# Optimization experiments

Measured on AMD Instinct MI355X. Metric: run time of the kernel, lower is better.

## Reference

```python
import jax, jax.numpy as jnp
import numpy as np

B, S, E = 2, 2048, 2048
H, D = 16, 128  # num_attention_heads, head_dim = hidden_size // num_heads


def rotate_half(x):
    x1 = x[..., : x.shape[-1] // 2]
    x2 = x[..., x.shape[-1] // 2 :]
    return jnp.concatenate((-x2, x1), axis=-1)


def setup_inputs() -> dict:
    key = jax.random.key(0)
    ks = jax.random.split(key, 7)
    return {
        "hidden_states": jax.random.normal(ks[0], (B, S, E), dtype=jnp.float32),
        "cos": jax.random.uniform(ks[1], (1, 1, S, D), dtype=jnp.float32),
        "sin": jax.random.uniform(ks[2], (1, 1, S, D), dtype=jnp.float32),
        "wq": jax.random.normal(ks[3], (E, H * D), dtype=jnp.float32) / np.sqrt(E),
        "wk": jax.random.normal(ks[4], (E, H * D), dtype=jnp.float32) / np.sqrt(E),
        "wv": jax.random.normal(ks[5], (E, H * D), dtype=jnp.float32) / np.sqrt(E),
        "wo": jax.random.normal(ks[6], (H * D, E), dtype=jnp.float32) / np.sqrt(H * D),
    }


def reference(hidden_states, cos, sin, wq, wk, wv, wo):
    # QKV projections (no bias, per attention_bias=False)
    q = (hidden_states @ wq).reshape(B, S, H, D).transpose(0, 2, 1, 3)  # bhsd
    k = (hidden_states @ wk).reshape(B, S, H, D).transpose(0, 2, 1, 3)
    v = (hidden_states @ wv).reshape(B, S, H, D).transpose(0, 2, 1, 3)
    # RoPE (applied after the head transpose, as in the original)
    q = q * cos + rotate_half(q) * sin
    k = k * cos + rotate_half(k) * sin
    # NOTE: original forward never applies self.scaling and uses no causal mask.
    scores = jnp.einsum("bhqd,bhkd->bhqk", q, k)
    attn = jax.nn.softmax(scores.astype(jnp.float32), axis=-1)
    out = jnp.einsum("bhqk,bhkd->bhqd", attn, v)
    out = out.transpose(0, 2, 1, 3).reshape(B, S, H * D)
    return out @ wo
```

## Files before the change

kernel.cpp:

```cpp
#include <hip/hip_runtime.h>
#include <stdint.h>

typedef _Float16 f16;
typedef _Float16 half8 __attribute__((ext_vector_type(8)));
typedef _Float16 half4 __attribute__((ext_vector_type(4)));
typedef __fp16 fp16x2 __attribute__((ext_vector_type(2)));
typedef float f32x4 __attribute__((ext_vector_type(4)));
typedef float f32x16 __attribute__((ext_vector_type(16)));
typedef uint32_t u32x4 __attribute__((ext_vector_type(4)));

static constexpr int Bsz = 2, S = 2048, E = 2048, H = 16, D = 128;
static constexpr int M = Bsz * S;
static constexpr int N_QKV = 3 * H * D;
static constexpr int HD = H * D;

__device__ __forceinline__ void gload_lds16(const void* gp, void* lp) {
  __builtin_amdgcn_global_load_lds(
      (const __attribute__((address_space(1))) uint32_t*)(uintptr_t)gp,
      (__attribute__((address_space(3))) uint32_t*)(uint32_t)(uintptr_t)lp,
      16, 0, 0);
}

__device__ __forceinline__ uint32_t pkrtz(float a, float b) {
  fp16x2 r = __builtin_amdgcn_cvt_pkrtz(a, b);
  return __builtin_bit_cast(uint32_t, r);
}

__global__ void cast_f32_f16(const float* __restrict__ in, f16* __restrict__ out) {
  size_t i = (size_t)(blockIdx.x * 256 + threadIdx.x) * 8;
  float4 a = *(const float4*)&in[i];
  float4 b = *(const float4*)&in[i + 4];
  half8 h;
  h[0] = (f16)a.x; h[1] = (f16)a.y; h[2] = (f16)a.z; h[3] = (f16)a.w;
  h[4] = (f16)b.x; h[5] = (f16)b.y; h[6] = (f16)b.z; h[7] = (f16)b.w;
  *(half8*)&out[i] = h;
}

__global__ void transpose_cast(const float* __restrict__ wq, const float* __restrict__ wk,
                               const float* __restrict__ wv, const float* __restrict__ wo,
                               f16* __restrict__ wt, f16* __restrict__ wot) {
  __shared__ float tile[32][33];
  int z = blockIdx.z;
  const float* src = (z == 0) ? wq : (z == 1) ? wk : (z == 2) ? wv : wo;
  f16* dst = (z == 3) ? wot : wt + (size_t)z * E * HD;
  int bx = blockIdx.x * 32, by = blockIdx.y * 32;
  int tx = threadIdx.x, ty = threadIdx.y;
#pragma unroll
  for (int r = 0; r < 4; ++r)
    tile[ty + r * 8][tx] = src[(size_t)(by + ty + r * 8) * 2048 + bx + tx];
  __syncthreads();
#pragma unroll
  for (int r = 0; r < 4; ++r)
    dst[(size_t)(bx + ty + r * 8) * 2048 + by + tx] = (f16)tile[tx][ty + r * 8];
}

#define ABUF(b_, kh_) ((b_) * 16384 + (kh_) * 8192)
#define BBUF(b_) (32768 + (b_) * 8192)
#define STAGE_A(T_, kh_)                                                     \
  do {                                                                       \
    int ko_ = (T_) * 64 + (kh_) * 32;                                        \
    int bb_ = (T_) & 1;                                                      \
    gload_lds16(Abase + ko_ + ca0, &lds[ABUF(bb_, kh_) + t * 8]);            \
    gload_lds16(Abase + ko_ + ca1, &lds[ABUF(bb_, kh_) + 4096 + t * 8]);     \
  } while (0)
#define STAGE_B(T_)                                                          \
  do {                                                                       \
    int ko_ = (T_) * 64;                                                     \
    int bb_ = (T_) & 1;                                                      \
    gload_lds16(Br0 + ko_, &lds[BBUF(bb_) + t * 8]);                         \
    gload_lds16(Br1 + ko_, &lds[BBUF(bb_) + 4096 + t * 8]);                  \
  } while (0)
#define LDA2(mq_, kh_)                                                       \
  _Pragma("unroll") for (int i2 = 0; i2 < 2; ++i2) {                         \
    int ra = wm * 64 + ((mq_)*2 + i2) * 16 + lr;                             \
    int s_ = g ^ ((ra >> 2) & 3);                                            \
    af[i2] = *(const half8*)&lds[ABUF(cb, kh_) + (s_ >> 1) * 4096 + ra * 16 + (s_ & 1) * 8]; \
  }
#define LDB_GEN(kh_, RB_)                                                    \
  _Pragma("unroll") for (int j = 0; j < 4; ++j) {                            \
    int rb = (RB_);                                                          \
    bf[j] = *(const half8*)&lds[BBUF(cb) + rb * 64 + ((((kh_)*4) + g) ^ (rb & 7)) * 8]; \
  }
#define MM8(mq_, SWAP_)                                                      \
  __builtin_amdgcn_s_setprio(1);                                             \
  _Pragma("unroll") for (int i2 = 0; i2 < 2; ++i2)                           \
  _Pragma("unroll") for (int j = 0; j < 4; ++j)                              \
      acc[(mq_)*2 + i2][j] = (SWAP_)                                         \
          ? __builtin_amdgcn_mfma_f32_16x16x32_f16(bf[j], af[i2], acc[(mq_)*2 + i2][j], 0, 0, 0) \
          : __builtin_amdgcn_mfma_f32_16x16x32_f16(af[i2], bf[j], acc[(mq_)*2 + i2][j], 0, 0, 0); \
  __builtin_amdgcn_s_setprio(0);
#define BAR() __builtin_amdgcn_s_barrier()
#define VM6() asm volatile("s_waitcnt vmcnt(6)" ::: "memory")
#define VM4() asm volatile("s_waitcnt vmcnt(4)" ::: "memory")
#define VM0() asm volatile("s_waitcnt vmcnt(0)" ::: "memory")

#define KLOOP(RB_, SWAP_)                                                    \
  for (int T = 0; T < 32; ++T) {                                             \
    const int cb = T & 1;                                                    \
    half8 af[2], bf[4];                                                      \
    LDB_GEN(0, RB_); LDA2(0, 0);                                             \
    if (T + 1 < 32) STAGE_A(T + 1, 1);                                       \
    BAR(); MM8(0, SWAP_); BAR();                                             \
    LDA2(1, 0);                                                              \
    if (T >= 29) { VM0(); } else { VM6(); }                                  \
    BAR(); MM8(1, SWAP_); BAR();                                             \
    LDB_GEN(1, RB_); LDA2(0, 1);                                             \
    if (T + 2 < 32) STAGE_A(T + 2, 0);                                       \
    BAR(); MM8(0, SWAP_); BAR();                                             \
    LDA2(1, 1);                                                              \
    if (T + 2 < 32) STAGE_B(T + 2);                                          \
    if (T >= 29) { VM0(); } else { VM6(); }                                  \
    BAR(); MM8(1, SWAP_); BAR();                                             \
  }

__global__ __launch_bounds__(512, 1) void qkv8(const f16* __restrict__ A,
                                               const f16* __restrict__ Bt,
                                               const float* __restrict__ cosb,
                                               const float* __restrict__ sinb,
                                               f16* __restrict__ Qb,
                                               f16* __restrict__ Kb,
                                               f16* __restrict__ VtG) {
  __shared__ f16 lds[49152];
  const int Kk = E;
  const int t = threadIdx.x, l = t & 63, wid = t >> 6;
  const int wm = wid >> 1, wn = wid & 1;
  const int lr = l & 15, g = l >> 4;
  const int bid = blockIdx.x;
  const int ii = bid >> 3;
  const int bm = (bid & 7) * 2 + (ii & 1);
  const int bn = ii >> 1;
  const int arow = t >> 1, ah = t & 1;
  const int fa = (arow >> 2) & 3;
  const int ca0 = (ah ^ fa) * 8;
  const int ca1 = ((2 | ah) ^ fa) * 8;
  const f16* Abase = A + (size_t)(bm * 256 + arow) * Kk;
  const int brl = t >> 3, bc = t & 7;
  const int cbx = (bc ^ (brl & 7)) * 8;
  const f16* Br0 = Bt + (size_t)(bn * 128 + brl) * Kk + cbx;
  const f16* Br1 = Bt + (size_t)(bn * 128 + 64 + brl) * Kk + cbx;
  const int bt = bn >> 4, h = bn & 15;
  const int bh = (bm >> 3) * 16 + h;
  const int sblk = (bm & 7) * 256;

  f32x4 acc[4][4] = {};
  STAGE_A(0, 0); STAGE_A(0, 1); STAGE_B(0);
  STAGE_A(1, 0); STAGE_B(1);
  VM4();
  BAR();

  if (bt < 2) {
    KLOOP(wn * 32 + (j & 1) * 16 + (j >> 1) * 64 + lr, true)
    f16* Dst = (bt == 0) ? Qb : Kb;
#pragma unroll
    for (int i = 0; i < 4; ++i) {
      const int s = sblk + wm * 64 + i * 16 + lr;
      const size_t obase = ((size_t)bh * S + s) * D;
      const size_t cbase = (size_t)s * D;
#pragma unroll
      for (int j = 0; j < 2; ++j) {
        const int dlo = wn * 32 + j * 16 + g * 4;
        float4 cl = *(const float4*)&cosb[cbase + dlo];
        float4 ch = *(const float4*)&cosb[cbase + dlo + 64];
        float4 sl = *(const float4*)&sinb[cbase + dlo];
        float4 sh = *(const float4*)&sinb[cbase + dlo + 64];
        float cla[4] = {cl.x, cl.y, cl.z, cl.w}, cha[4] = {ch.x, ch.y, ch.z, ch.w};
        float sla[4] = {sl.x, sl.y, sl.z, sl.w}, sha[4] = {sh.x, sh.y, sh.z, sh.w};
        half4 olo, ohi;
#pragma unroll
        for (int r = 0; r < 4; ++r) {
          float xl = acc[i][j][r], xh = acc[i][j + 2][r];
          olo[r] = (f16)(xl * cla[r] - xh * sla[r]);
          ohi[r] = (f16)(xh * cha[r] + xl * sha[r]);
        }
        *(half4*)&Dst[obase + dlo] = olo;
        *(half4*)&Dst[obase + dlo + 64] = ohi;
      }
    }
  } else {
    KLOOP(wn * 64 + j * 16 + lr, false)
#pragma unroll
    for (int j = 0; j < 4; ++j) {
      int d = wn * 64 + j * 16 + lr;
      size_t rowb = ((size_t)bh * D + d) * S;
#pragma unroll
      for (int i = 0; i < 4; ++i) {
        int s0 = sblk + wm * 64 + i * 16 + g * 4;
        half4 h4;
#pragma unroll
        for (int r = 0; r < 4; ++r) h4[r] = (f16)acc[i][j][r];
        *(half4*)&VtG[rowb + s0] = h4;
      }
    }
  }
}

__global__ __launch_bounds__(512, 1) void gemm8o(const f16* __restrict__ A,
                                                 const f16* __restrict__ Bt,
                                                 float* __restrict__ C) {
  __shared__ f16 lds[49152];
  const int Kk = HD;
  const int t = threadIdx.x, l = t & 63, wid = t >> 6;
  const int wm = wid >> 1, wn = wid & 1;
  const int lr = l & 15, g = l >> 4;
  const int bid = blockIdx.x;
  const int ii = bid >> 3;
  const int bm = (bid & 7) * 2 + (ii & 1);
  const int bn = ii >> 1;
  const int arow = t >> 1, ah = t & 1;
  const int fa = (arow >> 2) & 3;
  const int ca0 = (ah ^ fa) * 8;
  const int ca1 = ((2 | ah) ^ fa) * 8;
  const f16* Abase = A + (size_t)(bm * 256 + arow) * Kk;
  const int brl = t >> 3, bc = t & 7;
  const int cbx = (bc ^ (brl & 7)) * 8;
  const f16* Br0 = Bt + (size_t)(bn * 128 + brl) * Kk + cbx;
  const f16* Br1 = Bt + (size_t)(bn * 128 + 64 + brl) * Kk + cbx;

  f32x4 acc[4][4] = {};
  STAGE_A(0, 0); STAGE_A(0, 1); STAGE_B(0);
  STAGE_A(1, 0); STAGE_B(1);
  VM4();
  BAR();
  KLOOP(wn * 64 + j * 16 + lr, false)

#pragma unroll
  for (int i = 0; i < 4; ++i)
#pragma unroll
    for (int j = 0; j < 4; ++j) {
      int row = bm * 256 + wm * 64 + i * 16 + g * 4;
      int col = bn * 128 + wn * 64 + j * 16 + lr;
#pragma unroll
      for (int r = 0; r < 4; ++r)
        C[(size_t)(row + r) * E + col] = acc[i][j][r];
    }
}

__device__ __forceinline__ void stage_kv(const f16* __restrict__ Kg, const f16* __restrict__ Vg,
                                         f16* KsB, f16* VsB, int t, int kv) {
#pragma unroll
  for (int rnd = 0; rnd < 4; ++rnd) {
    int row = rnd * 16 + (t >> 4);
    int c = t & 15;
    gload_lds16(&Kg[(size_t)(kv + row) * D + ((c ^ (row & 7)) * 8)], &KsB[rnd * 2048 + t * 8]);
  }
#pragma unroll
  for (int rnd = 0; rnd < 4; ++rnd) {
    int row = rnd * 32 + (t >> 3);
    int c = t & 7;
    gload_lds16(&Vg[(size_t)row * S + kv + ((c ^ (row & 7)) * 8)], &VsB[rnd * 2048 + t * 8]);
  }
}

__global__ __launch_bounds__(256, 2) void flash_attn2(const f16* __restrict__ Q,
                                                      const f16* __restrict__ K,
                                                      const f16* __restrict__ Vt,
                                                      f16* __restrict__ O) {
  __shared__ f16 lds[2][16384];
  const int t = threadIdx.x, l = t & 63, w = t >> 6;
  const int c = l & 31, hi = l >> 5;
  int bid = blockIdx.x;
  bid = (bid & 7) * 64 + (bid >> 3);
  const int bh = bid >> 4, qt = bid & 15;
  const size_t baseQ = (size_t)bh * S * D;
  const f16* Kg = K + baseQ;
  const f16* Vg = Vt + (size_t)bh * D * S;
  const int q0 = qt * 128 + w * 32;
  half8 qf[8];
#pragma unroll
  for (int dc = 0; dc < 8; ++dc)
    qf[dc] = *(const half8*)&Q[baseQ + (size_t)(q0 + c) * D + dc * 16 + hi * 8];
  f32x16 o[4] = {};
  float m = -3.0e38f, ssum = 0.f;

  stage_kv(Kg, Vg, &lds[0][0], &lds[0][8192], t, 0);
  __syncthreads();

  for (int it = 0; it < S / 64; ++it) {
    const int cur = it & 1;
    const f16* KsB = &lds[cur][0];
    const f16* VsB = &lds[cur][8192];
    if (it + 1 < S / 64) stage_kv(Kg, Vg, &lds[cur ^ 1][0], &lds[cur ^ 1][8192], t, (it + 1) * 64);

    f32x16 s0 = {}, s1 = {};
    __builtin_amdgcn_s_setprio(1);
#pragma unroll
    for (int dc = 0; dc < 8; ++dc) {
      const int r0 = c, r1 = 32 + c;
      half8 kf0 = *(const half8*)&KsB[r0 * 128 + (((2 * dc + hi) ^ (r0 & 7)) * 8)];
      half8 kf1 = *(const half8*)&KsB[r1 * 128 + (((2 * dc + hi) ^ (r1 & 7)) * 8)];
      s0 = __builtin_amdgcn_mfma_f32_32x32x16_f16(kf0, qf[dc], s0, 0, 0, 0);
      s1 = __builtin_amdgcn_mfma_f32_32x32x16_f16(kf1, qf[dc], s1, 0, 0, 0);
    }
    __builtin_amdgcn_s_setprio(0);

    float tm = s0[0];
#pragma unroll
    for (int r = 1; r < 16; ++r) tm = fmaxf(tm, s0[r]);
#pragma unroll
    for (int r = 0; r < 16; ++r) tm = fmaxf(tm, s1[r]);
    tm = fmaxf(tm, __shfl_xor(tm, 32));
    if (!__all(tm <= m + 8.f)) {
      float mn = fmaxf(m, tm);
      float corr = __expf(m - mn);
      m = mn;
      ssum *= corr;
#pragma unroll
      for (int dt = 0; dt < 4; ++dt)
#pragma unroll
        for (int r = 0; r < 16; ++r) o[dt][r] *= corr;
    }
    float ts = 0.f;
#pragma unroll
    for (int r = 0; r < 16; ++r) { s0[r] = __expf(s0[r] - m); ts += s0[r]; }
#pragma unroll
    for (int r = 0; r < 16; ++r) { s1[r] = __expf(s1[r] - m); ts += s1[r]; }
    ts += __shfl_xor(ts, 32);
    ssum += ts;

    half8 pf[4];
#pragma unroll
    for (int ks = 0; ks < 4; ++ks) {
      const int B0 = 2 * (ks & 1), B1 = B0 + 1;
      uint32_t X0, X1, Y0, Y1;
      if (ks < 2) {
        X0 = pkrtz(s0[4 * B0 + 0], s0[4 * B0 + 1]);
        X1 = pkrtz(s0[4 * B0 + 2], s0[4 * B0 + 3]);
        Y0 = pkrtz(s0[4 * B1 + 0], s0[4 * B1 + 1]);
        Y1 = pkrtz(s0[4 * B1 + 2], s0[4 * B1 + 3]);
      } else {
        X0 = pkrtz(s1[4 * B0 + 0], s1[4 * B0 + 1]);
        X1 = pkrtz(s1[4 * B0 + 2], s1[4 * B0 + 3]);
        Y0 = pkrtz(s1[4 * B1 + 0], s1[4 * B1 + 1]);
        Y1 = pkrtz(s1[4 * B1 + 2], s1[4 * B1 + 3]);
      }
      asm volatile("v_permlane32_swap_b32 %0, %1" : "+v"(X0), "+v"(Y0));
      asm volatile("v_permlane32_swap_b32 %0, %1" : "+v"(X1), "+v"(Y1));
      u32x4 pw; pw[0] = X0; pw[1] = X1; pw[2] = Y0; pw[3] = Y1;
      pf[ks] = __builtin_bit_cast(half8, pw);
    }

    __builtin_amdgcn_s_setprio(1);
#pragma unroll
    for (int dt = 0; dt < 4; ++dt) {
      const int row = dt * 32 + c;
#pragma unroll
      for (int ks = 0; ks < 4; ++ks) {
        half8 vf = *(const half8*)&VsB[row * 64 + (((2 * ks + hi) ^ (row & 7)) * 8)];
        o[dt] = __builtin_amdgcn_mfma_f32_32x32x16_f16(vf, pf[ks], o[dt], 0, 0, 0);
      }
    }
    __builtin_amdgcn_s_setprio(0);
    __syncthreads();
  }

  const float inv = 1.f / ssum;
  const int b = bh >> 4, h = bh & 15;
  const size_t orow = ((size_t)(b * S + q0 + c)) * HD + h * D;
#pragma unroll
  for (int dt = 0; dt < 4; ++dt)
#pragma unroll
    for (int b2 = 0; b2 < 4; ++b2) {
      half4 h4;
#pragma unroll
      for (int a = 0; a < 4; ++a) h4[a] = (f16)(o[dt][4 * b2 + a] * inv);
      *(half4*)&O[orow + dt * 32 + 8 * b2 + 4 * hi] = h4;
    }
}

extern "C" void kernel_launch(void* const* d_in, const int* in_sizes, int n_in,
                              void* d_out, int out_size, void* d_ws, size_t ws_size,
                              hipStream_t stream) {
  (void)in_sizes; (void)n_in; (void)out_size; (void)ws_size;
  const float* hs = (const float*)d_in[0];
  const float* cosb = (const float*)d_in[1];
  const float* sinb = (const float*)d_in[2];
  const float* wq = (const float*)d_in[3];
  const float* wk = (const float*)d_in[4];
  const float* wv = (const float*)d_in[5];
  const float* wo = (const float*)d_in[6];
  float* out = (float*)d_out;
  char* ws = (char*)d_ws;
  f16* hs16 = (f16*)(ws);
  f16* attn = (f16*)(ws);
  f16* wt   = (f16*)(ws + (16u << 20));
  f16* wot  = (f16*)(ws + (40u << 20));
  f16* Qb   = (f16*)(ws + (48u << 20));
  f16* Kb   = (f16*)(ws + (64u << 20));
  f16* VtG  = (f16*)(ws + (80u << 20));

  cast_f32_f16<<<dim3(4096), dim3(256), 0, stream>>>(hs, hs16);
  transpose_cast<<<dim3(64, 64, 4), dim3(32, 8), 0, stream>>>(wq, wk, wv, wo, wt, wot);
  qkv8<<<dim3(768), dim3(512), 0, stream>>>(hs16, wt, cosb, sinb, Qb, Kb, VtG);
  flash_attn2<<<dim3(512), dim3(256), 0, stream>>>(Qb, Kb, VtG, attn);
  gemm8o<<<dim3(256), dim3(512), 0, stream>>>(attn, wot, out);
}
```

Before: 290.1 us.

## Widen QKV GEMM tiles to 256x256 and use simpler 128x128 output-projection GEMM

The QKV projection kernel now computes 256x256 output tiles per 512-thread block instead of 256x128. Each wave covers 128 rows by 64 columns, and the LDS B buffer is doubled. The RoPE and V-transpose epilogues are remapped so one tile spans two heads. The output projection replaces the pipelined 256x128 kernel with a templated 128x128 GEMM using 256 threads and four blocks per CU. That kernel uses a plain synchronous staging loop. The aim is more operand reuse per LDS load in QKV and better occupancy and grid fill for the output GEMM, at the cost of higher register and LDS pressure, only 384 QKV blocks, and no load/compute overlap in the new GEMM.

Result: no change. 284.6 us (-1.9%).

```diff
diff --git a/kernel.cpp b/kernel.cpp
--- a/kernel.cpp
+++ b/kernel.cpp
@@ -55,7 +55,7 @@
 }
 
 #define ABUF(b_, kh_) ((b_) * 16384 + (kh_) * 8192)
-#define BBUF(b_) (32768 + (b_) * 8192)
+#define BBUF(b_) (32768 + (b_) * 16384)
 #define STAGE_A(T_, kh_)                                                     \
   do {                                                                       \
     int ko_ = (T_) * 64 + (kh_) * 32;                                        \
@@ -69,66 +69,66 @@
     int bb_ = (T_) & 1;                                                      \
     gload_lds16(Br0 + ko_, &lds[BBUF(bb_) + t * 8]);                         \
     gload_lds16(Br1 + ko_, &lds[BBUF(bb_) + 4096 + t * 8]);                  \
+    gload_lds16(Br2 + ko_, &lds[BBUF(bb_) + 8192 + t * 8]);                  \
+    gload_lds16(Br3 + ko_, &lds[BBUF(bb_) + 12288 + t * 8]);                 \
   } while (0)
-#define LDA2(mq_, kh_)                                                       \
-  _Pragma("unroll") for (int i2 = 0; i2 < 2; ++i2) {                         \
-    int ra = wm * 64 + ((mq_)*2 + i2) * 16 + lr;                             \
+#define LDA4(mh_, kh_)                                                       \
+  _Pragma("unroll") for (int i2 = 0; i2 < 4; ++i2) {                         \
+    int ra = wm * 128 + ((mh_)*4 + i2) * 16 + lr;                            \
     int s_ = g ^ ((ra >> 2) & 3);                                            \
     af[i2] = *(const half8*)&lds[ABUF(cb, kh_) + (s_ >> 1) * 4096 + ra * 16 + (s_ & 1) * 8]; \
   }
-#define LDB_GEN(kh_, RB_)                                                    \
+#define LDB4(kh_, RB_)                                                       \
   _Pragma("unroll") for (int j = 0; j < 4; ++j) {                            \
     int rb = (RB_);                                                          \
     bf[j] = *(const half8*)&lds[BBUF(cb) + rb * 64 + ((((kh_)*4) + g) ^ (rb & 7)) * 8]; \
   }
-#define MM8(mq_, SWAP_)                                                      \
+#define MM16(mh_, SWAP_)                                                     \
   __builtin_amdgcn_s_setprio(1);                                             \
-  _Pragma("unroll") for (int i2 = 0; i2 < 2; ++i2)                           \
+  _Pragma("unroll") for (int i2 = 0; i2 < 4; ++i2)                           \
   _Pragma("unroll") for (int j = 0; j < 4; ++j)                              \
-      acc[(mq_)*2 + i2][j] = (SWAP_)                                         \
-          ? __builtin_amdgcn_mfma_f32_16x16x32_f16(bf[j], af[i2], acc[(mq_)*2 + i2][j], 0, 0, 0) \
-          : __builtin_amdgcn_mfma_f32_16x16x32_f16(af[i2], bf[j], acc[(mq_)*2 + i2][j], 0, 0, 0); \
+      acc[(mh_)*4 + i2][j] = (SWAP_)                                         \
+          ? __builtin_amdgcn_mfma_f32_16x16x32_f16(bf[j], af[i2], acc[(mh_)*4 + i2][j], 0, 0, 0) \
+          : __builtin_amdgcn_mfma_f32_16x16x32_f16(af[i2], bf[j], acc[(mh_)*4 + i2][j], 0, 0, 0); \
   __builtin_amdgcn_s_setprio(0);
 #define BAR() __builtin_amdgcn_s_barrier()
+#define VM8() asm volatile("s_waitcnt vmcnt(8)" ::: "memory")
 #define VM6() asm volatile("s_waitcnt vmcnt(6)" ::: "memory")
-#define VM4() asm volatile("s_waitcnt vmcnt(4)" ::: "memory")
 #define VM0() asm volatile("s_waitcnt vmcnt(0)" ::: "memory")
-
 #define KLOOP(RB_, SWAP_)                                                    \
   for (int T = 0; T < 32; ++T) {                                             \
     const int cb = T & 1;                                                    \
-    half8 af[2], bf[4];                                                      \
-    LDB_GEN(0, RB_); LDA2(0, 0);                                             \
+    half8 af[4], bf[4];                                                      \
+    LDB4(0, RB_); LDA4(0, 0);                                                \
     if (T + 1 < 32) STAGE_A(T + 1, 1);                                       \
-    BAR(); MM8(0, SWAP_); BAR();                                             \
-    LDA2(1, 0);                                                              \
-    if (T >= 29) { VM0(); } else { VM6(); }                                  \
-    BAR(); MM8(1, SWAP_); BAR();                                             \
-    LDB_GEN(1, RB_); LDA2(0, 1);                                             \
+    BAR(); MM16(0, SWAP_); BAR();                                            \
+    LDA4(1, 0);                                                              \
+    if (T >= 29) { VM0(); } else { VM8(); }                                  \
+    BAR(); MM16(1, SWAP_); BAR();                                            \
+    LDB4(1, RB_); LDA4(0, 1);                                                \
     if (T + 2 < 32) STAGE_A(T + 2, 0);                                       \
-    BAR(); MM8(0, SWAP_); BAR();                                             \
-    LDA2(1, 1);                                                              \
+    BAR(); MM16(0, SWAP_); BAR();                                            \
+    LDA4(1, 1);                                                              \
     if (T + 2 < 32) STAGE_B(T + 2);                                          \
-    if (T >= 29) { VM0(); } else { VM6(); }                                  \
-    BAR(); MM8(1, SWAP_); BAR();                                             \
-  }
-
-__global__ __launch_bounds__(512, 1) void qkv8(const f16* __restrict__ A,
-                                               const f16* __restrict__ Bt,
-                                               const float* __restrict__ cosb,
-                                               const float* __restrict__ sinb,
-                                               f16* __restrict__ Qb,
-                                               f16* __restrict__ Kb,
-                                               f16* __restrict__ VtG) {
-  __shared__ f16 lds[49152];
+    if (T >= 29) { VM0(); } else { VM8(); }                                  \
+    BAR(); MM16(1, SWAP_); BAR();                                            \
+  }
+
+__global__ __launch_bounds__(512, 1) void qkv256(const f16* __restrict__ A,
+                                                 const f16* __restrict__ Bt,
+                                                 const float* __restrict__ cosb,
+                                                 const float* __restrict__ sinb,
+                                                 f16* __restrict__ Qb,
+                                                 f16* __restrict__ Kb,
+                                                 f16* __restrict__ VtG) {
+  __shared__ f16 lds[65536];
   const int Kk = E;
   const int t = threadIdx.x, l = t & 63, wid = t >> 6;
-  const int wm = wid >> 1, wn = wid & 1;
+  const int wm = wid >> 2, wn = wid & 3;
   const int lr = l & 15, g = l >> 4;
   const int bid = blockIdx.x;
-  const int ii = bid >> 3;
-  const int bm = (bid & 7) * 2 + (ii & 1);
-  const int bn = ii >> 1;
+  const int bm = (bid & 7) * 2 + ((bid >> 3) & 1);
+  const int bn = bid >> 4;
   const int arow = t >> 1, ah = t & 1;
   const int fa = (arow >> 2) & 3;
   const int ca0 = (ah ^ fa) * 8;
@@ -136,39 +136,43 @@
   const f16* Abase = A + (size_t)(bm * 256 + arow) * Kk;
   const int brl = t >> 3, bc = t & 7;
   const int cbx = (bc ^ (brl & 7)) * 8;
-  const f16* Br0 = Bt + (size_t)(bn * 128 + brl) * Kk + cbx;
-  const f16* Br1 = Bt + (size_t)(bn * 128 + 64 + brl) * Kk + cbx;
-  const int bt = bn >> 4, h = bn & 15;
-  const int bh = (bm >> 3) * 16 + h;
+  const f16* Br0 = Bt + (size_t)(bn * 256 + brl) * Kk + cbx;
+  const f16* Br1 = Bt + (size_t)(bn * 256 + 64 + brl) * Kk + cbx;
+  const f16* Br2 = Bt + (size_t)(bn * 256 + 128 + brl) * Kk + cbx;
+  const f16* Br3 = Bt + (size_t)(bn * 256 + 192 + brl) * Kk + cbx;
+  const int bt = bn >> 3;
+  const int h0 = (bn & 7) * 2;
+  const int b = bm >> 3;
   const int sblk = (bm & 7) * 256;
 
-  f32x4 acc[4][4] = {};
+  f32x4 acc[8][4] = {};
   STAGE_A(0, 0); STAGE_A(0, 1); STAGE_B(0);
   STAGE_A(1, 0); STAGE_B(1);
-  VM4();
+  VM6();
   BAR();
 
   if (bt < 2) {
-    KLOOP(wn * 32 + (j & 1) * 16 + (j >> 1) * 64 + lr, true)
+    KLOOP(wn * 16 + ((j & 1) << 6) + ((j >> 1) << 7) + lr, true)
     f16* Dst = (bt == 0) ? Qb : Kb;
 #pragma unroll
-    for (int i = 0; i < 4; ++i) {
-      const int s = sblk + wm * 64 + i * 16 + lr;
-      const size_t obase = ((size_t)bh * S + s) * D;
+    for (int mi = 0; mi < 8; ++mi) {
+      const int s = sblk + wm * 128 + mi * 16 + lr;
       const size_t cbase = (size_t)s * D;
-#pragma unroll
-      for (int j = 0; j < 2; ++j) {
-        const int dlo = wn * 32 + j * 16 + g * 4;
-        float4 cl = *(const float4*)&cosb[cbase + dlo];
-        float4 ch = *(const float4*)&cosb[cbase + dlo + 64];
-        float4 sl = *(const float4*)&sinb[cbase + dlo];
-        float4 sh = *(const float4*)&sinb[cbase + dlo + 64];
-        float cla[4] = {cl.x, cl.y, cl.z, cl.w}, cha[4] = {ch.x, ch.y, ch.z, ch.w};
-        float sla[4] = {sl.x, sl.y, sl.z, sl.w}, sha[4] = {sh.x, sh.y, sh.z, sh.w};
+      const int dlo = wn * 16 + g * 4;
+      float4 cl = *(const float4*)&cosb[cbase + dlo];
+      float4 ch = *(const float4*)&cosb[cbase + dlo + 64];
+      float4 sl = *(const float4*)&sinb[cbase + dlo];
+      float4 sh = *(const float4*)&sinb[cbase + dlo + 64];
+      float cla[4] = {cl.x, cl.y, cl.z, cl.w}, cha[4] = {ch.x, ch.y, ch.z, ch.w};
+      float sla[4] = {sl.x, sl.y, sl.z, sl.w}, sha[4] = {sh.x, sh.y, sh.z, sh.w};
+#pragma unroll
+      for (int jh = 0; jh < 2; ++jh) {
+        const int bh = b * 16 + h0 + jh;
+        const size_t obase = ((size_t)bh * S + s) * D;
         half4 olo, ohi;
 #pragma unroll
         for (int r = 0; r < 4; ++r) {
-          float xl = acc[i][j][r], xh = acc[i][j + 2][r];
+          float xl = acc[mi][2 * jh][r], xh = acc[mi][2 * jh + 1][r];
           olo[r] = (f16)(xl * cla[r] - xh * sla[r]);
           ohi[r] = (f16)(xh * cha[r] + xl * sha[r]);
         }
@@ -180,58 +184,89 @@
     KLOOP(wn * 64 + j * 16 + lr, false)
 #pragma unroll
     for (int j = 0; j < 4; ++j) {
-      int d = wn * 64 + j * 16 + lr;
-      size_t rowb = ((size_t)bh * D + d) * S;
-#pragma unroll
-      for (int i = 0; i < 4; ++i) {
-        int s0 = sblk + wm * 64 + i * 16 + g * 4;
+      const int cv = (bn & 7) * 256 + wn * 64 + j * 16 + lr;
+      const int h = cv >> 7, d = cv & 127;
+      const size_t rowb = ((size_t)(b * 16 + h) * D + d) * S;
+#pragma unroll
+      for (int mi = 0; mi < 8; ++mi) {
+        const int s0 = sblk + wm * 128 + mi * 16 + g * 4;
         half4 h4;
 #pragma unroll
-        for (int r = 0; r < 4; ++r) h4[r] = (f16)acc[i][j][r];
+        for (int r = 0; r < 4; ++r) h4[r] = (f16)acc[mi][j][r];
         *(half4*)&VtG[rowb + s0] = h4;
       }
     }
   }
 }
-
-__global__ __launch_bounds__(512, 1) void gemm8o(const f16* __restrict__ A,
-                                                 const f16* __restrict__ Bt,
-                                                 float* __restrict__ C) {
-  __shared__ f16 lds[49152];
-  const int Kk = HD;
-  const int t = threadIdx.x, l = t & 63, wid = t >> 6;
-  const int wm = wid >> 1, wn = wid & 1;
+#undef ABUF
+#undef BBUF
+#undef STAGE_A
+#undef STAGE_B
+#undef LDA4
+#undef LDB4
+#undef MM16
+#undef KLOOP
+#undef VM8
+#undef VM6
+#undef VM0
+#undef BAR
+
+#define STAGE4(PTR, BASE, KOFF, DST)                                       \
+  gload_lds16(&PTR[BASE + (KOFF) + scol], &DST[t * 8]);                    \
+  gload_lds16(&PTR[BASE + (size_t)64 * Kk + (KOFF) + scol], &DST[2048 + t * 8]);
+
+template <typename OutT>
+__global__ __launch_bounds__(256, 4) void gemm_bt(const f16* __restrict__ A,
+                                                  const f16* __restrict__ Bt,
+                                                  OutT* __restrict__ C,
+                                                  int Nn, int Kk) {
+  __shared__ f16 As[8192];
+  __shared__ f16 Bs[8192];
+  const int t = threadIdx.x, l = t & 63;
+  const int wm = (t >> 7) & 1, wn = (t >> 6) & 1;
+  const int bid = blockIdx.x;
+  const int bm = (bid & 7) * 4 + ((bid >> 3) & 3);
+  const int bn = bid >> 5;
   const int lr = l & 15, g = l >> 4;
-  const int bid = blockIdx.x;
-  const int ii = bid >> 3;
-  const int bm = (bid & 7) * 2 + (ii & 1);
-  const int bn = ii >> 1;
-  const int arow = t >> 1, ah = t & 1;
-  const int fa = (arow >> 2) & 3;
-  const int ca0 = (ah ^ fa) * 8;
-  const int ca1 = ((2 | ah) ^ fa) * 8;
-  const f16* Abase = A + (size_t)(bm * 256 + arow) * Kk;
-  const int brl = t >> 3, bc = t & 7;
-  const int cbx = (bc ^ (brl & 7)) * 8;
-  const f16* Br0 = Bt + (size_t)(bn * 128 + brl) * Kk + cbx;
-  const f16* Br1 = Bt + (size_t)(bn * 128 + 64 + brl) * Kk + cbx;
-
+  const int srow = t >> 2;
+  const int scol = (((t & 3) ^ (srow & 3)) * 8);
+  const size_t abase = (size_t)(bm * 128 + srow) * Kk;
+  const size_t bbase = (size_t)(bn * 128 + srow) * Kk;
   f32x4 acc[4][4] = {};
-  STAGE_A(0, 0); STAGE_A(0, 1); STAGE_B(0);
-  STAGE_A(1, 0); STAGE_B(1);
-  VM4();
-  BAR();
-  KLOOP(wn * 64 + j * 16 + lr, false)
-
+  for (int k0 = 0; k0 < Kk; k0 += 64) {
+    __syncthreads();
+    STAGE4(A, abase, k0, As);
+    STAGE4(Bt, bbase, k0, Bs);
+    STAGE4(A, abase, k0 + 32, (As + 4096));
+    STAGE4(Bt, bbase, k0 + 32, (Bs + 4096));
+    __syncthreads();
+#pragma unroll
+    for (int kh = 0; kh < 2; ++kh) {
+      const int so = kh * 4096;
+      half8 af[4], bf[4];
+#pragma unroll
+      for (int i = 0; i < 4; ++i) {
+        int ra = wm * 64 + i * 16 + lr;
+        int rb = wn * 64 + i * 16 + lr;
+        af[i] = *(const half8*)&As[so + ra * 32 + ((g ^ (ra & 3)) * 8)];
+        bf[i] = *(const half8*)&Bs[so + rb * 32 + ((g ^ (rb & 3)) * 8)];
+      }
+#pragma unroll
+      for (int i = 0; i < 4; ++i)
+#pragma unroll
+        for (int j = 0; j < 4; ++j)
+          acc[i][j] = __builtin_amdgcn_mfma_f32_16x16x32_f16(af[i], bf[j], acc[i][j], 0, 0, 0);
+    }
+  }
 #pragma unroll
   for (int i = 0; i < 4; ++i)
 #pragma unroll
     for (int j = 0; j < 4; ++j) {
-      int row = bm * 256 + wm * 64 + i * 16 + g * 4;
+      int row = bm * 128 + wm * 64 + i * 16 + g * 4;
       int col = bn * 128 + wn * 64 + j * 16 + lr;
 #pragma unroll
       for (int r = 0; r < 4; ++r)
-        C[(size_t)(row + r) * E + col] = acc[i][j][r];
+        C[(size_t)(row + r) * Nn + col] = (OutT)acc[i][j][r];
     }
 }
 
@@ -390,7 +425,7 @@
 
   cast_f32_f16<<<dim3(4096), dim3(256), 0, stream>>>(hs, hs16);
   transpose_cast<<<dim3(64, 64, 4), dim3(32, 8), 0, stream>>>(wq, wk, wv, wo, wt, wot);
-  qkv8<<<dim3(768), dim3(512), 0, stream>>>(hs16, wt, cosb, sinb, Qb, Kb, VtG);
+  qkv256<<<dim3(384), dim3(512), 0, stream>>>(hs16, wt, cosb, sinb, Qb, Kb, VtG);
   flash_attn2<<<dim3(512), dim3(256), 0, stream>>>(Qb, Kb, VtG, attn);
-  gemm8o<<<dim3(256), dim3(512), 0, stream>>>(attn, wot, out);
-}
+  gemm_bt<float><<<dim3(512), dim3(256), 0, stream>>>(attn, wot, out, E, HD);
+}
```
